# Optimization experiments

Measured on AMD Instinct MI355X. Metric: run time of the kernel, lower is better.

The kernel has to match this reference:

```python
import jax, jax.numpy as jnp
import numpy as np

B, S, IN, OUT = 4, 2048, 4096, 16384

def setup_inputs() -> dict:
    key = jax.random.key(0)
    k1, k2, k3, k4 = jax.random.split(key, 4)
    x = jax.random.normal(k1, (B, S, IN), dtype=jnp.float32)
    weight_int = jax.random.randint(k2, (OUT, IN), -128, 128, dtype=jnp.int32)
    # per-row scale, small positive values as produced by quantize_weight
    weight_scale = jax.random.uniform(k3, (OUT, 1), dtype=jnp.float32, minval=1e-3, maxval=2e-2)
    weight_zero_point = jnp.zeros((OUT, 1), dtype=jnp.int32)  # symmetric quantization
    bias = jax.random.normal(k4, (OUT,), dtype=jnp.float32) * 0.02
    return {"x": x, "weight_int": weight_int, "weight_scale": weight_scale,
            "weight_zero_point": weight_zero_point, "bias": bias}

def reference(x, weight_int, weight_scale, weight_zero_point, bias):
    # Dequantize: (int8 - zero_point) * per-row scale -> fp32 weight [OUT, IN]
    weight_fp = (weight_int.astype(jnp.float32) - weight_zero_point.astype(jnp.float32)) * weight_scale
    # F.linear: x @ W^T + b
    out = jnp.einsum('bsi,oi->bso', x, weight_fp) + bias
    return out
```

## Files before the change

kernel.cpp:

```cpp
#include <hip/hip_runtime.h>
#include <hip/hip_bf16.h>

typedef __bf16 bf16x8 __attribute__((ext_vector_type(8)));
typedef float  f32x4  __attribute__((ext_vector_type(4)));
typedef int    i32x4  __attribute__((ext_vector_type(4)));

#define BM 128
#define BN 128
#define BK 128
#define THREADS 256

__device__ __forceinline__ void gload_lds16(const void* g, void* l) {
  __builtin_amdgcn_global_load_lds(
      (const __attribute__((address_space(1))) void*)g,
      (__attribute__((address_space(3))) void*)l, 16, 0, 0);
}

__device__ __forceinline__ void vmwait0() { asm volatile("s_waitcnt vmcnt(0)"); }

__device__ __forceinline__ void tile_barrier() {
  __builtin_amdgcn_sched_barrier(0);
  asm volatile("s_barrier");
  __builtin_amdgcn_sched_barrier(0);
}

__global__ __launch_bounds__(256)
void prep_kernel(const float* __restrict__ x, signed char* __restrict__ xq,
                 float* __restrict__ sx, int* __restrict__ rowsum,
                 const int* __restrict__ w, const int* __restrict__ zp,
                 signed char* __restrict__ wq, int M, int K) {
  const int tid = threadIdx.x;
  if ((int)blockIdx.x < M) {
    const int row = blockIdx.x;
    const int wave = tid >> 6, lane = tid & 63;
    const float* xr = x + (long)row * K;
    __shared__ float smax[4];
    __shared__ int   ssum[4];

    float amax = 0.f;
    for (int i = tid * 16; i < K; i += 256 * 16) {
      #pragma unroll
      for (int j = 0; j < 4; ++j) {
        float4 v = *(const float4*)(xr + i + j * 4);
        amax = fmaxf(amax, fmaxf(fmaxf(fabsf(v.x), fabsf(v.y)),
                                 fmaxf(fabsf(v.z), fabsf(v.w))));
      }
    }
    #pragma unroll
    for (int m = 32; m >= 1; m >>= 1) amax = fmaxf(amax, __shfl_xor(amax, m));
    if (lane == 0) smax[wave] = amax;
    __syncthreads();
    const float m4 = fmaxf(fmaxf(smax[0], smax[1]), fmaxf(smax[2], smax[3]));
    const float scale = (m4 > 0.f) ? (m4 / 127.f) : 1.f;
    const float inv   = (m4 > 0.f) ? (127.f / m4) : 0.f;

    int lsum = 0;
    for (int i = tid * 16; i < K; i += 256 * 16) {
      union { signed char c[16]; int4 v; } u;
      #pragma unroll
      for (int j = 0; j < 4; ++j) {
        float4 v = *(const float4*)(xr + i + j * 4);
        int q0 = __float2int_rn(v.x * inv), q1 = __float2int_rn(v.y * inv);
        int q2 = __float2int_rn(v.z * inv), q3 = __float2int_rn(v.w * inv);
        u.c[j*4+0] = (signed char)q0; u.c[j*4+1] = (signed char)q1;
        u.c[j*4+2] = (signed char)q2; u.c[j*4+3] = (signed char)q3;
        lsum += q0 + q1 + q2 + q3;
      }
      *(int4*)(xq + (long)row * K + i) = u.v;
    }
    #pragma unroll
    for (int m = 32; m >= 1; m >>= 1) lsum += __shfl_xor(lsum, m);
    if (lane == 0) ssum[wave] = lsum;
    __syncthreads();
    if (tid == 0) {
      rowsum[row] = ssum[0] + ssum[1] + ssum[2] + ssum[3];
      sx[row] = scale;
    }
  } else {
    const long i = ((long)(blockIdx.x - M) * 4096) + tid * 16;
    const int z = zp[i / K];
    union { signed char c[16]; int4 v; } u;
    #pragma unroll
    for (int j = 0; j < 4; ++j) {
      int4 a = *(const int4*)(w + i + j * 4);
      int q0 = min(127, max(-128, a.x - z)), q1 = min(127, max(-128, a.y - z));
      int q2 = min(127, max(-128, a.z - z)), q3 = min(127, max(-128, a.w - z));
      u.c[j*4+0] = (signed char)q0; u.c[j*4+1] = (signed char)q1;
      u.c[j*4+2] = (signed char)q2; u.c[j*4+3] = (signed char)q3;
    }
    *(int4*)(wq + i) = u.v;
  }
}

__global__ __launch_bounds__(THREADS, 3)
void qlin_gemm_i8(const signed char* __restrict__ A, const signed char* __restrict__ B,
                  const float* __restrict__ sx, const int* __restrict__ rowsum,
                  const int* __restrict__ zp,
                  const float* __restrict__ scale, const float* __restrict__ bias,
                  float* __restrict__ C, int M, int N, int K) {
  __shared__ alignas(16) signed char As[BM * BK];
  __shared__ alignas(16) signed char Bs[BN * BK];

  const int tid  = threadIdx.x;
  const int wave = tid >> 6;
  const int lane = tid & 63;
  const int wm = wave >> 1, wn = wave & 1;

  const int bid = blockIdx.x, nwg = gridDim.x;
  const int ntn = N / BN, ntm = M / BM;
  long tm, tn;
  if ((nwg & 7) == 0 && (ntm & 7) == 0 && (ntn & 7) == 0 &&
      (nwg >> 3) == (ntm >> 3) * ntn) {
    const int xcd = bid & 7;
    const int l   = bid >> 3;
    const int R   = ntm >> 3;
    const int ps  = R << 3;
    const int w   = l % ps;
    tm = (long)xcd * R + (w % R);
    tn = (long)(l / ps) * 8 + (w / R);
  } else {
    tm = bid / ntn; tn = bid % ntn;
  }
  const long row0 = tm * BM;
  const long col0 = tn * BN;

  const signed char* Ag = A + row0 * (long)K;
  const signed char* Bg = B + col0 * (long)K;

  const int srow = wave * 8 + (lane >> 3);
  const int kswz = ((lane & 7) ^ (lane >> 3)) * 16;

#define STAGE_A(c, kt) gload_lds16(Ag + (long)((c)*32 + srow) * K + (kt) + kswz, \
                                   &As[(c)*4096 + wave*1024])
#define STAGE_B(c, kt) gload_lds16(Bg + (long)((c)*32 + srow) * K + (kt) + kswz, \
                                   &Bs[(c)*4096 + wave*1024])
#define STAGE8(kt) { STAGE_B(0,kt); STAGE_B(1,kt); STAGE_B(2,kt); STAGE_B(3,kt); \
                     STAGE_A(0,kt); STAGE_A(1,kt); STAGE_A(2,kt); STAGE_A(3,kt); }

  const int rsel = lane & 15;
  const int ksl  = lane >> 4;
  const int lan7 = lane & 7;

  i32x4 acc[4][4] = {};
  i32x4 bf[4][2];

#define AF_READ(m, kk)                                                          \
  (*(const i32x4*)&As[(wm*64 + (m)*16 + rsel)*BK                                \
                      + (((((kk)<<2)+ksl) ^ lan7) << 4)])

  const int NT = K / BK;

  for (int t = 0; t < NT; ++t) {
    const long kt = (long)t * BK;
    STAGE8(kt)
    vmwait0();
    tile_barrier();

    __builtin_amdgcn_s_setprio(1);
    #pragma unroll
    for (int n = 0; n < 4; ++n)
      #pragma unroll
      for (int kk = 0; kk < 2; ++kk)
        bf[n][kk] = *(const i32x4*)&Bs[(wn*64 + n*16 + rsel)*BK
                                       + ((((kk<<2)+ksl) ^ lan7) << 4)];
    i32x4 afp0, afp1;
    afp0 = AF_READ(0, 0);
    #pragma unroll
    for (int f = 0; f < 8; ++f) {
      const int m = f & 3, kk = f >> 2;
      if (f < 7) {
        const int m2 = (f + 1) & 3, kk2 = (f + 1) >> 2;
        if (f & 1) afp0 = AF_READ(m2, kk2);
        else       afp1 = AF_READ(m2, kk2);
      }
      #pragma unroll
      for (int n = 0; n < 4; ++n)
        acc[m][n] = __builtin_amdgcn_mfma_i32_16x16x64_i8(
            (f & 1) ? afp1 : afp0, bf[n][kk], acc[m][n], 0, 0, 0);
    }
    __builtin_amdgcn_s_setprio(0);
    tile_barrier();
  }
#undef AF_READ
#undef STAGE8
#undef STAGE_A
#undef STAGE_B

  float swv[4], bvv[4]; int zpv[4];
  #pragma unroll
  for (int n = 0; n < 4; ++n) {
    const long gcol = col0 + wn * 64 + n * 16 + rsel;
    swv[n] = scale[gcol];
    bvv[n] = bias[gcol];
    zpv[n] = zp[gcol];
  }
  #pragma unroll
  for (int m = 0; m < 4; ++m) {
    const long growb = row0 + wm * 64 + m * 16 + ksl * 4;
    #pragma unroll
    for (int j = 0; j < 4; ++j) {
      const long grow = growb + j;
      const float sxv = sx[grow];
      const int   rsv = rowsum[grow];
      float* orow = C + grow * (long)N;
      #pragma unroll
      for (int n = 0; n < 4; ++n) {
        const long gcol = col0 + wn * 64 + n * 16 + rsel;
        orow[gcol] = (float)(acc[m][n][j] - zpv[n] * rsv) * (sxv * swv[n]) + bvv[n];
      }
    }
  }
}

__global__ __launch_bounds__(256)
void qlin_gemm_small(const float* __restrict__ Af, const int* __restrict__ Bi,
                     const int* __restrict__ zp,
                     const float* __restrict__ scale, const float* __restrict__ bias,
                     float* __restrict__ C, int M, int N, int K) {
  __shared__ alignas(16) __bf16 As[128 * 64];
  __shared__ alignas(16) __bf16 Bs[128 * 64];
  const int tid = threadIdx.x, wave = tid >> 6, lane = tid & 63;
  int bid = blockIdx.x, nwg = gridDim.x, swz = bid;
  if ((nwg & 7) == 0) swz = (bid & 7) * (nwg >> 3) + (bid >> 3);
  const int ntn = N / 128;
  const long row0 = (long)(swz / ntn) * 128, col0 = (long)(swz % ntn) * 128;
  const int wr = wave >> 1, wc = wave & 1;
  f32x4 acc[4][4] = {};
  for (int kt = 0; kt < K; kt += 64) {
    #pragma unroll
    for (int i = 0; i < 4; ++i) {
      const int flat = i * 2048 + tid * 8;
      const int r = flat >> 6, cc = flat & 63;
      const int wcc = ((cc >> 3) ^ (r & 7)) << 3;
      const float* g = Af + (row0 + r) * (long)K + kt + cc;
      float4 f0 = *(const float4*)g; float4 f1 = *(const float4*)(g + 4);
      bf16x8 v;
      v[0]=(__bf16)f0.x; v[1]=(__bf16)f0.y; v[2]=(__bf16)f0.z; v[3]=(__bf16)f0.w;
      v[4]=(__bf16)f1.x; v[5]=(__bf16)f1.y; v[6]=(__bf16)f1.z; v[7]=(__bf16)f1.w;
      *(bf16x8*)(As + r * 64 + wcc) = v;
    }
    #pragma unroll
    for (int i = 0; i < 4; ++i) {
      const int flat = i * 2048 + tid * 8;
      const int r = flat >> 6, cc = flat & 63;
      const int wcc = ((cc >> 3) ^ (r & 7)) << 3;
      const long grow = col0 + r;
      const int z = zp[grow];
      const int* g = Bi + grow * (long)K + kt + cc;
      int4 a = *(const int4*)g; int4 b = *(const int4*)(g + 4);
      bf16x8 v;
      v[0]=(__bf16)(float)(a.x-z); v[1]=(__bf16)(float)(a.y-z);
      v[2]=(__bf16)(float)(a.z-z); v[3]=(__bf16)(float)(a.w-z);
      v[4]=(__bf16)(float)(b.x-z); v[5]=(__bf16)(float)(b.y-z);
      v[6]=(__bf16)(float)(b.z-z); v[7]=(__bf16)(float)(b.w-z);
      *(bf16x8*)(Bs + r * 64 + wcc) = v;
    }
    __syncthreads();
    #pragma unroll
    for (int kk = 0; kk < 2; ++kk) {
      bf16x8 af[4], bfr[4];
      const int rs = lane & 15, ks = kk * 4 + (lane >> 4);
      const int rd = (ks ^ (lane & 7)) << 3;
      #pragma unroll
      for (int m = 0; m < 4; ++m) af[m] = *(const bf16x8*)(As + (wr*64 + m*16 + rs)*64 + rd);
      #pragma unroll
      for (int n = 0; n < 4; ++n) bfr[n] = *(const bf16x8*)(Bs + (wc*64 + n*16 + rs)*64 + rd);
      #pragma unroll
      for (int m = 0; m < 4; ++m)
        #pragma unroll
        for (int n = 0; n < 4; ++n)
          acc[m][n] = __builtin_amdgcn_mfma_f32_16x16x32_bf16(af[m], bfr[n], acc[m][n], 0, 0, 0);
    }
    __syncthreads();
  }
  #pragma unroll
  for (int m = 0; m < 4; ++m) {
    const long grow = row0 + wr * 64 + m * 16 + ((lane >> 4) << 2);
    #pragma unroll
    for (int n = 0; n < 4; ++n) {
      const long gcol = col0 + wc * 64 + n * 16 + (lane & 15);
      const float s = scale[gcol], bb2 = bias[gcol];
      float* o = C + grow * (long)N + gcol;
      #pragma unroll
      for (int j = 0; j < 4; ++j) o[(long)j * N] = acc[m][n][j] * s + bb2;
    }
  }
}

extern "C" void kernel_launch(void* const* d_in, const int* in_sizes, int n_in,
                              void* d_out, int out_size, void* d_ws, size_t ws_size,
                              hipStream_t stream) {
  const float* x    = (const float*)d_in[0];
  const int*   wint = (const int*)d_in[1];
  const float* wsc  = (const float*)d_in[2];
  const int*   wzp  = (const int*)d_in[3];
  const float* bias = (const float*)d_in[4];
  float* out = (float*)d_out;

  const int N = in_sizes[4];
  const int K = in_sizes[1] / N;
  const int M = in_sizes[0] / K;

  const size_t xqb = (size_t)M * K;
  const size_t wqb = (size_t)N * K;
  const size_t sxb = (size_t)M * sizeof(float);
  const size_t rsb = (size_t)M * sizeof(int);
  const int NT = K / BK;
  const long nk = (long)N * K;

  if (ws_size >= xqb + wqb + sxb + rsb && (M % BM) == 0 && (N % BN) == 0 &&
      (K % BK) == 0 && (K % 4096) == 0 && NT >= 2 && (nk % 4096) == 0) {
    signed char* xq = (signed char*)d_ws;
    signed char* wq = xq + xqb;
    float* sx  = (float*)(wq + wqb);
    int* rsum  = (int*)((char*)sx + sxb);
    const int wblocks = (int)(nk / 4096);
    prep_kernel<<<M + wblocks, 256, 0, stream>>>(x, xq, sx, rsum,
                                                 wint, wzp, wq, M, K);
    const int grid = (M / BM) * (N / BN);
    qlin_gemm_i8<<<grid, THREADS, 0, stream>>>(xq, wq, sx, rsum, wzp, wsc, bias,
                                               out, M, N, K);
  } else {
    const int grid = (M / 128) * (N / 128);
    qlin_gemm_small<<<grid, 256, 0, stream>>>(x, wint, wzp, wsc, bias, out, M, N, K);
  }
}
```

Baseline: 690.0 us.

## Split K tile into two 64-wide LDS halves and overlap loads with compute

```diff
diff --git a/kernel.cpp b/kernel.cpp
--- a/kernel.cpp
+++ b/kernel.cpp
@@ -7,7 +7,6 @@
 
 #define BM 128
 #define BN 128
-#define BK 128
 #define THREADS 256
 
 __device__ __forceinline__ void gload_lds16(const void* g, void* l) {
@@ -16,7 +15,10 @@
       (__attribute__((address_space(3))) void*)l, 16, 0, 0);
 }
 
-__device__ __forceinline__ void vmwait0() { asm volatile("s_waitcnt vmcnt(0)"); }
+template<int N> __device__ __forceinline__ void vmwait() {
+  if constexpr (N == 0)      asm volatile("s_waitcnt vmcnt(0)");
+  else if constexpr (N == 4) asm volatile("s_waitcnt vmcnt(4)");
+}
 
 __device__ __forceinline__ void tile_barrier() {
   __builtin_amdgcn_sched_barrier(0);
@@ -98,8 +100,8 @@
                   const int* __restrict__ zp,
                   const float* __restrict__ scale, const float* __restrict__ bias,
                   float* __restrict__ C, int M, int N, int K) {
-  __shared__ alignas(16) signed char As[BM * BK];
-  __shared__ alignas(16) signed char Bs[BN * BK];
+  __shared__ alignas(16) signed char As[2][BM * 64];
+  __shared__ alignas(16) signed char Bs[2][BN * 64];
 
   const int tid  = threadIdx.x;
   const int wave = tid >> 6;
@@ -127,62 +129,77 @@
   const signed char* Ag = A + row0 * (long)K;
   const signed char* Bg = B + col0 * (long)K;
 
-  const int srow = wave * 8 + (lane >> 3);
-  const int kswz = ((lane & 7) ^ (lane >> 3)) * 16;
-
-#define STAGE_A(c, kt) gload_lds16(Ag + (long)((c)*32 + srow) * K + (kt) + kswz, \
-                                   &As[(c)*4096 + wave*1024])
-#define STAGE_B(c, kt) gload_lds16(Bg + (long)((c)*32 + srow) * K + (kt) + kswz, \
-                                   &Bs[(c)*4096 + wave*1024])
-#define STAGE8(kt) { STAGE_B(0,kt); STAGE_B(1,kt); STAGE_B(2,kt); STAGE_B(3,kt); \
-                     STAGE_A(0,kt); STAGE_A(1,kt); STAGE_A(2,kt); STAGE_A(3,kt); }
+  const int srow = lane >> 2;
+  const int kswz = ((lane & 3) ^ ((lane >> 3) & 3)) * 16;
+
+#define STAGE_A(h, c, kt) gload_lds16(                                        \
+    Ag + (long)(32*wave + 16*(c) + srow) * K + (kt) + (h)*64 + kswz,          \
+    &As[h][2048*wave + 1024*(c)])
+#define STAGE_B(h, c, kt) gload_lds16(                                        \
+    Bg + (long)(32*wave + 16*(c) + srow) * K + (kt) + (h)*64 + kswz,          \
+    &Bs[h][2048*wave + 1024*(c)])
+#define STAGE4(h, kt) { STAGE_A(h,0,kt); STAGE_A(h,1,kt); \
+                        STAGE_B(h,0,kt); STAGE_B(h,1,kt); }
 
   const int rsel = lane & 15;
   const int ksl  = lane >> 4;
-  const int lan7 = lane & 7;
+  const int rdx  = ((ksl ^ ((rsel >> 1) & 3)) << 4);
 
   i32x4 acc[4][4] = {};
-  i32x4 bf[4][2];
-
-#define AF_READ(m, kk)                                                          \
-  (*(const i32x4*)&As[(wm*64 + (m)*16 + rsel)*BK                                \
-                      + (((((kk)<<2)+ksl) ^ lan7) << 4)])
-
-  const int NT = K / BK;
-
-  for (int t = 0; t < NT; ++t) {
-    const long kt = (long)t * BK;
-    STAGE8(kt)
-    vmwait0();
+
+#define AF_READ(h, m) \
+  (*(const i32x4*)&As[h][(wm*64 + (m)*16 + rsel)*64 + rdx])
+
+#define COMPUTE(h)                                                             \
+  {                                                                            \
+    __builtin_amdgcn_s_setprio(1);                                             \
+    i32x4 bf[4];                                                               \
+    _Pragma("unroll")                                                          \
+    for (int n = 0; n < 4; ++n)                                                \
+      bf[n] = *(const i32x4*)&Bs[h][(wn*64 + n*16 + rsel)*64 + rdx];           \
+    i32x4 afp0, afp1;                                                          \
+    afp0 = AF_READ(h, 0);                                                      \
+    _Pragma("unroll")                                                          \
+    for (int f = 0; f < 4; ++f) {                                              \
+      if (f < 3) {                                                             \
+        if (f & 1) afp0 = AF_READ(h, f + 1);                                   \
+        else       afp1 = AF_READ(h, f + 1);                                   \
+      }                                                                        \
+      _Pragma("unroll")                                                        \
+      for (int n = 0; n < 4; ++n)                                              \
+        acc[f][n] = __builtin_amdgcn_mfma_i32_16x16x64_i8(                     \
+            (f & 1) ? afp1 : afp0, bf[n], acc[f][n], 0, 0, 0);                 \
+    }                                                                          \
+    __builtin_amdgcn_s_setprio(0);                                             \
+  }
+
+  const int NP = K / 128;
+
+  STAGE4(0, 0)
+  STAGE4(1, 0)
+  vmwait<4>();
+  tile_barrier();
+
+  for (int p = 0; p < NP - 1; ++p) {
+    const long ktn = (long)(p + 1) * 128;
+    COMPUTE(0)
     tile_barrier();
-
-    __builtin_amdgcn_s_setprio(1);
-    #pragma unroll
-    for (int n = 0; n < 4; ++n)
-      #pragma unroll
-      for (int kk = 0; kk < 2; ++kk)
-        bf[n][kk] = *(const i32x4*)&Bs[(wn*64 + n*16 + rsel)*BK
-                                       + ((((kk<<2)+ksl) ^ lan7) << 4)];
-    i32x4 afp0, afp1;
-    afp0 = AF_READ(0, 0);
-    #pragma unroll
-    for (int f = 0; f < 8; ++f) {
-      const int m = f & 3, kk = f >> 2;
-      if (f < 7) {
-        const int m2 = (f + 1) & 3, kk2 = (f + 1) >> 2;
-        if (f & 1) afp0 = AF_READ(m2, kk2);
-        else       afp1 = AF_READ(m2, kk2);
-      }
-      #pragma unroll
-      for (int n = 0; n < 4; ++n)
-        acc[m][n] = __builtin_amdgcn_mfma_i32_16x16x64_i8(
-            (f & 1) ? afp1 : afp0, bf[n][kk], acc[m][n], 0, 0, 0);
-    }
-    __builtin_amdgcn_s_setprio(0);
+    STAGE4(0, ktn)
+    vmwait<4>();
     tile_barrier();
-  }
+    COMPUTE(1)
+    tile_barrier();
+    STAGE4(1, ktn)
+    vmwait<4>();
+    tile_barrier();
+  }
+  COMPUTE(0)
+  vmwait<0>();
+  tile_barrier();
+  COMPUTE(1)
+#undef COMPUTE
 #undef AF_READ
-#undef STAGE8
+#undef STAGE4
 #undef STAGE_A
 #undef STAGE_B
 
@@ -305,11 +322,10 @@
   const size_t wqb = (size_t)N * K;
   const size_t sxb = (size_t)M * sizeof(float);
   const size_t rsb = (size_t)M * sizeof(int);
-  const int NT = K / BK;
   const long nk = (long)N * K;
 
   if (ws_size >= xqb + wqb + sxb + rsb && (M % BM) == 0 && (N % BN) == 0 &&
-      (K % BK) == 0 && (K % 4096) == 0 && NT >= 2 && (nk % 4096) == 0) {
+      (K % 128) == 0 && (K % 4096) == 0 && (K / 128) >= 2 && (nk % 4096) == 0) {
     signed char* xq = (signed char*)d_ws;
     signed char* wq = xq + xqb;
     float* sx  = (float*)(wq + wqb);
```

After: 834.1 us. 1.21x slower.
